# Kernel optimization log

Measured on AMD Instinct MI355X. Metric: run time of the kernel, lower is better.

The kernel has to match this reference:

```python
import jax, jax.numpy as jnp
import numpy as np

BN_EPS = 1e-5


def setup_inputs() -> dict:
    key = jax.random.key(0)
    ks = jax.random.split(key, 4)
    S, B, F, P, T, H, W = 4, 2, 64, 16, 32, 64, 64
    HID = 32
    feats = jax.random.normal(ks[0], (S, B, F, T, H, W), dtype=jnp.float32)
    p_s = jax.random.normal(ks[1], (B, P, T, H, W), dtype=jnp.float32)
    w1 = jax.random.normal(ks[2], (HID, F + P), dtype=jnp.float32) * (1.0 / np.sqrt(F + P))
    w2 = jax.random.normal(ks[3], (HID,), dtype=jnp.float32) * (1.0 / np.sqrt(HID))
    return {
        "feats": feats,
        "p_s": p_s,
        "w1": w1,
        "bn_gamma": jnp.ones((HID,), jnp.float32),
        "bn_beta": jnp.zeros((HID,), jnp.float32),
        "bn_mean": jnp.zeros((HID,), jnp.float32),
        "bn_var": jnp.ones((HID,), jnp.float32),
        "w2": w2,
        "b2": jnp.zeros((1,), jnp.float32),
    }


def reference(feats, p_s, w1, bn_gamma, bn_beta, bn_mean, bn_var, w2, b2):
    # feats: [S,B,F,T,H,W]; p_s: [B,P,T,H,W]
    F = feats.shape[2]
    w1_f, w1_p = w1[:, :F], w1[:, F:]
    # 1x1x1 conv on concat([f, p_s]) == split contraction; avoids materializing concat
    h = jnp.einsum('of,sbfthw->sbothw', w1_f, feats) \
        + jnp.einsum('op,bpthw->bothw', w1_p, p_s)[None]
    # BatchNorm3d (inference form) folded to scale/shift, then ReLU
    scale = bn_gamma / jnp.sqrt(bn_var + BN_EPS)
    shift = bn_beta - bn_mean * scale
    h = jax.nn.relu(h * scale[:, None, None, None] + shift[:, None, None, None])
    # second 1x1x1 conv: hidden -> 1 logit per branch
    logits = jnp.einsum('sbothw,o->sbthw', h, w2) + b2[0]
    alpha = jax.nn.softmax(logits, axis=0)            # softmax over branches S
    out = jnp.einsum('sbfthw,sbthw->bfthw', feats, alpha)
    return out, jnp.moveaxis(alpha, 0, 1)             # out:[B,F,T,H,W], alpha:[B,S,T,H,W]
```

## Files before the change

kernel.cpp:

```cpp
#include <hip/hip_runtime.h>
#include <hip/hip_bf16.h>
#include <stdint.h>

#define THW   131072
#define NS    4
#define NB    2
#define NF    64
#define NP    16
#define HID   32
#define BN_EPS 1e-5f
#define PXT   128

typedef short  bf16x8  __attribute__((ext_vector_type(8)));
typedef float  f32x16  __attribute__((ext_vector_type(16)));

union FragU { uint32_t u[4]; bf16x8 v; uint4 q; };

__device__ __forceinline__ uint32_t pk2(float a, float b) {
    __hip_bfloat162 h = __float22bfloat162_rn(make_float2(a, b));
    uint32_t r;
    __builtin_memcpy(&r, &h, sizeof(r));
    return r;
}
__device__ __forceinline__ float lo16(uint32_t u) { return __builtin_bit_cast(float, u << 16); }
__device__ __forceinline__ float hi16(uint32_t u) { return __builtin_bit_cast(float, u & 0xFFFF0000u); }

__device__ __forceinline__ void glds16(const float* g, void* l) {
    __builtin_amdgcn_global_load_lds(
        (const __attribute__((address_space(1))) uint32_t*)g,
        (__attribute__((address_space(3))) uint32_t*)l, 16, 0, 0);
}

__global__ __launch_bounds__(256, 2) void gssm_kernel(
    const float* __restrict__ feats, const float* __restrict__ ps,
    const float* __restrict__ w1,    const float* __restrict__ gamma,
    const float* __restrict__ beta,  const float* __restrict__ mean,
    const float* __restrict__ var,   const float* __restrict__ w2,
    float* __restrict__ out)
{
    __shared__ __align__(16) float    fbuf[2][NF][PXT];
    __shared__ __align__(16) float    pbuf[NP][PXT];
    __shared__ __align__(16) uint32_t w1lds[32 * 44];
    __shared__ float2 tbl[HID];

    const int tid  = threadIdx.x;
    const int lane = tid & 63;
    const int wv   = tid >> 6;
    const int hi   = lane >> 5;
    const int ln   = lane & 31;

    for (int t = tid; t < 1280; t += 256) {
        float2 v = ((const float2*)w1)[t];
        int o = t / 40, cp = t - o * 40;
        float sc = gamma[o] * rsqrtf(var[o] + BN_EPS);
        w1lds[o * 44 + (cp >> 3) * 8 + (cp & 7)] = pk2(v.x * sc, v.y * sc);
    }
    if (tid < HID) {
        float sc = gamma[tid] * rsqrtf(var[tid] + BN_EPS);
        tbl[tid] = make_float2(beta[tid] - mean[tid] * sc, w2[tid]);
    }

    const int px0g = blockIdx.x * PXT;
    const int b    = px0g >> 17;
    const int px0  = px0g & (THW - 1);

    const float* featsb = feats + (long)b * NF * THW + px0;
    const float* psb    = ps    + (long)b * NP * THW + px0;
    const long   sstr   = (long)NB * NF * THW;

    const long pl_off = (long)(lane >> 5) * THW + (ln << 2);
    const int  f0     = wv * 16;

    auto stage_feats = [&](int s, int buf) {
        const float* base = featsb + (long)s * sstr;
        #pragma unroll
        for (int i = 0; i < 8; ++i) {
            int f = f0 + i * 2;
            glds16(base + (long)f * THW + pl_off, (void*)&fbuf[buf][f][0]);
        }
    };

    {
        #pragma unroll
        for (int i = 0; i < 2; ++i) {
            int p = wv * 4 + i * 2;
            glds16(psb + (long)p * THW + pl_off, (void*)&pbuf[p][0]);
        }
    }
    stage_feats(0, 0);
    asm volatile("s_waitcnt vmcnt(0) lgkmcnt(0)" ::: "memory");
    __builtin_amdgcn_s_barrier();

    FragU afr[5];
    {
        const uint32_t abase = (uint32_t)(ln * 44 + hi * 4);
        #pragma unroll
        for (int k = 0; k < 5; ++k)
            afr[k].q = *((const uint4*)&w1lds[abase + k * 8]);
    }
    float sh[16], wo[16];
    #pragma unroll
    for (int r = 0; r < 16; ++r) {
        float2 t = tbl[(r & 3) + 8 * (r >> 2) + 4 * hi];
        sh[r] = t.x;
        wo[r] = t.y;
    }

    const int pxloc = wv * 32 + ln;

    FragU bp;
    #pragma unroll
    for (int r = 0; r < 4; ++r)
        bp.u[r] = pk2(pbuf[hi * 8 + 2 * r][pxloc], pbuf[hi * 8 + 2 * r + 1][pxloc]);

    auto consume = [&](int buf, FragU* pk) -> float {
        #pragma unroll
        for (int kb = 0; kb < 4; ++kb)
            #pragma unroll
            for (int r = 0; r < 4; ++r)
                pk[kb].u[r] = pk2(fbuf[buf][kb * 16 + hi * 8 + 2 * r][pxloc],
                                  fbuf[buf][kb * 16 + hi * 8 + 2 * r + 1][pxloc]);
        f32x16 acc;
        #pragma unroll
        for (int r = 0; r < 16; ++r) acc[r] = 0.f;
        acc = __builtin_amdgcn_mfma_f32_32x32x16_bf16(afr[4].v, bp.v,    acc, 0, 0, 0);
        acc = __builtin_amdgcn_mfma_f32_32x32x16_bf16(afr[0].v, pk[0].v, acc, 0, 0, 0);
        acc = __builtin_amdgcn_mfma_f32_32x32x16_bf16(afr[1].v, pk[1].v, acc, 0, 0, 0);
        acc = __builtin_amdgcn_mfma_f32_32x32x16_bf16(afr[2].v, pk[2].v, acc, 0, 0, 0);
        acc = __builtin_amdgcn_mfma_f32_32x32x16_bf16(afr[3].v, pk[3].v, acc, 0, 0, 0);
        float pp[4] = {0.f, 0.f, 0.f, 0.f};
        #pragma unroll
        for (int r = 0; r < 16; ++r) {
            float h = fmaxf(acc[r] + sh[r], 0.f);
            pp[r & 3] = fmaf(h, wo[r], pp[r & 3]);
        }
        float part = (pp[0] + pp[1]) + (pp[2] + pp[3]);
        return part + __shfl_xor(part, 32);
    };

    FragU pk0[4], pk1[4], pk2f[4], pk3[4];
    float lg0, lg1, lg2, lg3;

    stage_feats(1, 1);
    asm volatile("s_waitcnt vmcnt(8)" ::: "memory");
    __builtin_amdgcn_s_barrier();
    lg0 = consume(0, pk0);
    __builtin_amdgcn_s_barrier();

    stage_feats(2, 0);
    asm volatile("s_waitcnt vmcnt(8)" ::: "memory");
    __builtin_amdgcn_s_barrier();
    lg1 = consume(1, pk1);
    __builtin_amdgcn_s_barrier();

    stage_feats(3, 1);
    asm volatile("s_waitcnt vmcnt(8)" ::: "memory");
    __builtin_amdgcn_s_barrier();
    lg2 = consume(0, pk2f);
    __builtin_amdgcn_s_barrier();

    asm volatile("s_waitcnt vmcnt(0)" ::: "memory");
    __builtin_amdgcn_s_barrier();
    lg3 = consume(1, pk3);

    const float m   = fmaxf(fmaxf(lg0, lg1), fmaxf(lg2, lg3));
    const float e0  = __expf(lg0 - m), e1 = __expf(lg1 - m);
    const float e2  = __expf(lg2 - m), e3 = __expf(lg3 - m);
    const float inv = 1.f / (e0 + e1 + e2 + e3);
    const float a0 = e0 * inv, a1 = e1 * inv, a2 = e2 * inv, a3 = e3 * inv;

    const int thw = px0 + pxloc;

    float* ob = out + ((long)(b * NF + hi * 8)) * THW + thw;
    #pragma unroll
    for (int k = 0; k < 4; ++k)
        #pragma unroll
        for (int r = 0; r < 4; ++r) {
            float vlo = a0 * lo16(pk0[k].u[r]);
            float vhi = a0 * hi16(pk0[k].u[r]);
            vlo = fmaf(a1, lo16(pk1[k].u[r]), vlo);
            vhi = fmaf(a1, hi16(pk1[k].u[r]), vhi);
            vlo = fmaf(a2, lo16(pk2f[k].u[r]), vlo);
            vhi = fmaf(a2, hi16(pk2f[k].u[r]), vhi);
            vlo = fmaf(a3, lo16(pk3[k].u[r]), vlo);
            vhi = fmaf(a3, hi16(pk3[k].u[r]), vhi);
            ob[(long)(k * 16 + 2 * r)     * THW] = vlo;
            ob[(long)(k * 16 + 2 * r + 1) * THW] = vhi;
        }

    float* ab = out + (long)NB * NF * THW + ((long)(b * NS + hi * 2)) * THW + thw;
    ab[0]   = hi ? a2 : a0;
    ab[THW] = hi ? a3 : a1;
}

extern "C" void kernel_launch(void* const* d_in, const int* in_sizes, int n_in,
                              void* d_out, int out_size, void* d_ws, size_t ws_size,
                              hipStream_t stream) {
    const float* feats = (const float*)d_in[0];
    const float* ps    = (const float*)d_in[1];
    const float* w1    = (const float*)d_in[2];
    const float* gamma = (const float*)d_in[3];
    const float* beta  = (const float*)d_in[4];
    const float* mean  = (const float*)d_in[5];
    const float* var   = (const float*)d_in[6];
    const float* w2    = (const float*)d_in[7];
    float* out = (float*)d_out;

    dim3 grid(2048), block(256);
    hipLaunchKernelGGL(gssm_kernel, grid, block, 0, stream,
                       feats, ps, w1, gamma, beta, mean, var, w2, out);
}
```

Measured before the change: 92.21 us.

## Process four pixel tiles per block with cross-tile prefetch of next inputs

Result: faster. 80.10 us (-13.1%).

```diff
diff --git a/kernel.cpp b/kernel.cpp
--- a/kernel.cpp
+++ b/kernel.cpp
@@ -10,6 +10,7 @@
 #define HID   32
 #define BN_EPS 1e-5f
 #define PXT   128
+#define TPB   4
 
 typedef short  bf16x8  __attribute__((ext_vector_type(8)));
 typedef float  f32x16  __attribute__((ext_vector_type(16)));
@@ -59,36 +60,37 @@
         float sc = gamma[tid] * rsqrtf(var[tid] + BN_EPS);
         tbl[tid] = make_float2(beta[tid] - mean[tid] * sc, w2[tid]);
     }
-
-    const int px0g = blockIdx.x * PXT;
-    const int b    = px0g >> 17;
-    const int px0  = px0g & (THW - 1);
-
-    const float* featsb = feats + (long)b * NF * THW + px0;
-    const float* psb    = ps    + (long)b * NP * THW + px0;
-    const long   sstr   = (long)NB * NF * THW;
-
+    asm volatile("s_waitcnt vmcnt(0)" ::: "memory");
+
+    const int base9 = (int)(__brev((unsigned)blockIdx.x) >> 23);
+    const long sstr = (long)NB * NF * THW;
     const long pl_off = (long)(lane >> 5) * THW + (ln << 2);
     const int  f0     = wv * 16;
 
-    auto stage_feats = [&](int s, int buf) {
-        const float* base = featsb + (long)s * sstr;
+    auto tile_b   = [&](int t) { return (4 * base9 + t) >> 10; };
+    auto tile_px0 = [&](int t) { return ((4 * base9 + t) * PXT) & (THW - 1); };
+
+    auto stage_feats = [&](int t, int s, int buf) {
+        const float* base = feats + (long)tile_b(t) * NF * THW + tile_px0(t)
+                          + (long)s * sstr;
         #pragma unroll
         for (int i = 0; i < 8; ++i) {
             int f = f0 + i * 2;
             glds16(base + (long)f * THW + pl_off, (void*)&fbuf[buf][f][0]);
         }
     };
-
-    {
+    auto stage_p = [&](int t) {
+        const float* base = ps + (long)tile_b(t) * NP * THW + tile_px0(t);
         #pragma unroll
         for (int i = 0; i < 2; ++i) {
             int p = wv * 4 + i * 2;
-            glds16(psb + (long)p * THW + pl_off, (void*)&pbuf[p][0]);
-        }
-    }
-    stage_feats(0, 0);
-    asm volatile("s_waitcnt vmcnt(0) lgkmcnt(0)" ::: "memory");
+            glds16(base + (long)p * THW + pl_off, (void*)&pbuf[p][0]);
+        }
+    };
+
+    stage_p(0);
+    stage_feats(0, 0, 0);
+    asm volatile("s_waitcnt lgkmcnt(0)" ::: "memory");
     __builtin_amdgcn_s_barrier();
 
     FragU afr[5];
@@ -101,18 +103,14 @@
     float sh[16], wo[16];
     #pragma unroll
     for (int r = 0; r < 16; ++r) {
-        float2 t = tbl[(r & 3) + 8 * (r >> 2) + 4 * hi];
-        sh[r] = t.x;
-        wo[r] = t.y;
+        float2 t2 = tbl[(r & 3) + 8 * (r >> 2) + 4 * hi];
+        sh[r] = t2.x;
+        wo[r] = t2.y;
     }
 
     const int pxloc = wv * 32 + ln;
 
     FragU bp;
-    #pragma unroll
-    for (int r = 0; r < 4; ++r)
-        bp.u[r] = pk2(pbuf[hi * 8 + 2 * r][pxloc], pbuf[hi * 8 + 2 * r + 1][pxloc]);
-
     auto consume = [&](int buf, FragU* pk) -> float {
         #pragma unroll
         for (int kb = 0; kb < 4; ++kb)
@@ -128,69 +126,83 @@
         acc = __builtin_amdgcn_mfma_f32_32x32x16_bf16(afr[1].v, pk[1].v, acc, 0, 0, 0);
         acc = __builtin_amdgcn_mfma_f32_32x32x16_bf16(afr[2].v, pk[2].v, acc, 0, 0, 0);
         acc = __builtin_amdgcn_mfma_f32_32x32x16_bf16(afr[3].v, pk[3].v, acc, 0, 0, 0);
-        float pp[4] = {0.f, 0.f, 0.f, 0.f};
+        float pp4[4] = {0.f, 0.f, 0.f, 0.f};
         #pragma unroll
         for (int r = 0; r < 16; ++r) {
             float h = fmaxf(acc[r] + sh[r], 0.f);
-            pp[r & 3] = fmaf(h, wo[r], pp[r & 3]);
-        }
-        float part = (pp[0] + pp[1]) + (pp[2] + pp[3]);
+            pp4[r & 3] = fmaf(h, wo[r], pp4[r & 3]);
+        }
+        float part = (pp4[0] + pp4[1]) + (pp4[2] + pp4[3]);
         return part + __shfl_xor(part, 32);
     };
 
-    FragU pk0[4], pk1[4], pk2f[4], pk3[4];
-    float lg0, lg1, lg2, lg3;
-
-    stage_feats(1, 1);
-    asm volatile("s_waitcnt vmcnt(8)" ::: "memory");
-    __builtin_amdgcn_s_barrier();
-    lg0 = consume(0, pk0);
-    __builtin_amdgcn_s_barrier();
-
-    stage_feats(2, 0);
-    asm volatile("s_waitcnt vmcnt(8)" ::: "memory");
-    __builtin_amdgcn_s_barrier();
-    lg1 = consume(1, pk1);
-    __builtin_amdgcn_s_barrier();
-
-    stage_feats(3, 1);
-    asm volatile("s_waitcnt vmcnt(8)" ::: "memory");
-    __builtin_amdgcn_s_barrier();
-    lg2 = consume(0, pk2f);
-    __builtin_amdgcn_s_barrier();
-
-    asm volatile("s_waitcnt vmcnt(0)" ::: "memory");
-    __builtin_amdgcn_s_barrier();
-    lg3 = consume(1, pk3);
-
-    const float m   = fmaxf(fmaxf(lg0, lg1), fmaxf(lg2, lg3));
-    const float e0  = __expf(lg0 - m), e1 = __expf(lg1 - m);
-    const float e2  = __expf(lg2 - m), e3 = __expf(lg3 - m);
-    const float inv = 1.f / (e0 + e1 + e2 + e3);
-    const float a0 = e0 * inv, a1 = e1 * inv, a2 = e2 * inv, a3 = e3 * inv;
-
-    const int thw = px0 + pxloc;
-
-    float* ob = out + ((long)(b * NF + hi * 8)) * THW + thw;
-    #pragma unroll
-    for (int k = 0; k < 4; ++k)
-        #pragma unroll
-        for (int r = 0; r < 4; ++r) {
-            float vlo = a0 * lo16(pk0[k].u[r]);
-            float vhi = a0 * hi16(pk0[k].u[r]);
-            vlo = fmaf(a1, lo16(pk1[k].u[r]), vlo);
-            vhi = fmaf(a1, hi16(pk1[k].u[r]), vhi);
-            vlo = fmaf(a2, lo16(pk2f[k].u[r]), vlo);
-            vhi = fmaf(a2, hi16(pk2f[k].u[r]), vhi);
-            vlo = fmaf(a3, lo16(pk3[k].u[r]), vlo);
-            vhi = fmaf(a3, hi16(pk3[k].u[r]), vhi);
-            ob[(long)(k * 16 + 2 * r)     * THW] = vlo;
-            ob[(long)(k * 16 + 2 * r + 1) * THW] = vhi;
-        }
-
-    float* ab = out + (long)NB * NF * THW + ((long)(b * NS + hi * 2)) * THW + thw;
-    ab[0]   = hi ? a2 : a0;
-    ab[THW] = hi ? a3 : a1;
+    for (int t = 0; t < TPB; ++t) {
+        FragU pk0[4], pk1[4], pk2f[4], pk3[4];
+        float lg0, lg1, lg2, lg3;
+
+        stage_feats(t, 1, 1);
+        asm volatile("s_waitcnt vmcnt(8)" ::: "memory");
+        __builtin_amdgcn_s_barrier();
+        #pragma unroll
+        for (int r = 0; r < 4; ++r)
+            bp.u[r] = pk2(pbuf[hi * 8 + 2 * r][pxloc], pbuf[hi * 8 + 2 * r + 1][pxloc]);
+        lg0 = consume(0, pk0);
+        __builtin_amdgcn_s_barrier();
+
+        stage_feats(t, 2, 0);
+        asm volatile("s_waitcnt vmcnt(8)" ::: "memory");
+        __builtin_amdgcn_s_barrier();
+        lg1 = consume(1, pk1);
+        __builtin_amdgcn_s_barrier();
+
+        stage_feats(t, 3, 1);
+        asm volatile("s_waitcnt vmcnt(8)" ::: "memory");
+        __builtin_amdgcn_s_barrier();
+        lg2 = consume(0, pk2f);
+        __builtin_amdgcn_s_barrier();
+
+        if (t + 1 < TPB) {
+            stage_p(t + 1);
+            stage_feats(t + 1, 0, 0);
+            asm volatile("s_waitcnt vmcnt(10)" ::: "memory");
+        } else {
+            asm volatile("s_waitcnt vmcnt(0)" ::: "memory");
+        }
+        __builtin_amdgcn_s_barrier();
+        lg3 = consume(1, pk3);
+
+        const float m   = fmaxf(fmaxf(lg0, lg1), fmaxf(lg2, lg3));
+        const float e0  = __expf(lg0 - m), e1 = __expf(lg1 - m);
+        const float e2  = __expf(lg2 - m), e3 = __expf(lg3 - m);
+        const float inv = 1.f / (e0 + e1 + e2 + e3);
+        const float a0 = e0 * inv, a1 = e1 * inv, a2 = e2 * inv, a3 = e3 * inv;
+
+        const int b   = tile_b(t);
+        const int thw = tile_px0(t) + pxloc;
+
+        float* ob = out + ((long)(b * NF + hi * 8)) * THW + thw;
+        #pragma unroll
+        for (int k = 0; k < 4; ++k)
+            #pragma unroll
+            for (int r = 0; r < 4; ++r) {
+                float vlo = a0 * lo16(pk0[k].u[r]);
+                float vhi = a0 * hi16(pk0[k].u[r]);
+                vlo = fmaf(a1, lo16(pk1[k].u[r]), vlo);
+                vhi = fmaf(a1, hi16(pk1[k].u[r]), vhi);
+                vlo = fmaf(a2, lo16(pk2f[k].u[r]), vlo);
+                vhi = fmaf(a2, hi16(pk2f[k].u[r]), vhi);
+                vlo = fmaf(a3, lo16(pk3[k].u[r]), vlo);
+                vhi = fmaf(a3, hi16(pk3[k].u[r]), vhi);
+                ob[(long)(k * 16 + 2 * r)     * THW] = vlo;
+                ob[(long)(k * 16 + 2 * r + 1) * THW] = vhi;
+            }
+
+        float* ab = out + (long)NB * NF * THW + ((long)(b * NS + hi * 2)) * THW + thw;
+        ab[0]   = hi ? a2 : a0;
+        ab[THW] = hi ? a3 : a1;
+
+        __builtin_amdgcn_s_barrier();
+    }
 }
 
 extern "C" void kernel_launch(void* const* d_in, const int* in_sizes, int n_in,
@@ -206,7 +218,7 @@
     const float* w2    = (const float*)d_in[7];
     float* out = (float*)d_out;
 
-    dim3 grid(2048), block(256);
+    dim3 grid(512), block(256);
     hipLaunchKernelGGL(gssm_kernel, grid, block, 0, stream,
                        feats, ps, w1, gamma, beta, mean, var, w2, out);
 }
```
